# Kernel tuning notes

Hardware: AMD Instinct MI355X
Metric: run time of the kernel (lower is better)

## Reference

```python
import jax, jax.numpy as jnp
import numpy as np

N = 50000      # num nodes
E = 800000     # num edges (avg degree 16)
D = 128        # feature dim
HOP = 2        # number of propagation hops
FILL = 0.5     # self-loop fill value (A_hat = A + fill*I)


def setup_inputs() -> dict:
    key = jax.random.key(0)
    k1, k2, k3, k4, k5 = jax.random.split(key, 5)
    x_s = jax.random.normal(k1, (N, D), dtype=jnp.float32)
    x_t = jax.random.normal(k2, (N, D), dtype=jnp.float32)
    src = jax.random.randint(k3, (E,), 0, N)
    # guarantee no pre-existing self-loops so that appending all self-loops
    # exactly matches add_remaining_self_loops
    dst = (src + jax.random.randint(k4, (E,), 1, N)) % N
    edge_index = jnp.stack([src, dst]).astype(jnp.int32)
    edge_weight = jax.random.uniform(k5, (E,), dtype=jnp.float32)
    # DIMPA parameters, initialized to 1.0 per _reset_parameters
    w_s = jnp.ones((HOP + 1, 1), dtype=jnp.float32)
    w_t = jnp.ones((HOP + 1, 1), dtype=jnp.float32)
    return {"x_s": x_s, "x_t": x_t, "edge_index": edge_index,
            "edge_weight": edge_weight, "w_s": w_s, "w_t": w_t}


def _conv(x, row, col, w, n, fill):
    # Conv_Base: add self loops with weight `fill`, row-normalize by weighted
    # out-degree of `row`, scatter-add messages w_norm * x[row] onto `col`.
    loop = jnp.arange(n, dtype=row.dtype)
    row_a = jnp.concatenate([row, loop])
    col_a = jnp.concatenate([col, loop])
    w_a = jnp.concatenate([w, jnp.full((n,), fill, dtype=w.dtype)])
    deg = jax.ops.segment_sum(w_a, row_a, num_segments=n)
    deg_inv = jnp.where(deg == 0, jnp.zeros_like(deg), 1.0 / deg)  # inf -> 0
    w_norm = deg_inv[row_a] * w_a                                   # [E+n]
    return jax.ops.segment_sum(w_norm[:, None] * x[row_a], col_a, num_segments=n)


def reference(x_s, x_t, edge_index, edge_weight, w_s, w_t):
    n = x_s.shape[0]
    row, col = edge_index[0], edge_index[1]
    feat_s = w_s[0] * x_s
    feat_t = w_t[0] * x_t
    curr_s, curr_t = x_s, x_t
    for h in range(1, HOP + 1):
        curr_s = _conv(curr_s, row, col, edge_weight, n, FILL)
        # edge_index_t = edge_index[[1, 0]] -> swap row/col
        curr_t = _conv(curr_t, col, row, edge_weight, n, FILL)
        feat_s = feat_s + w_s[h] * curr_s
        feat_t = feat_t + w_t[h] * curr_t
    return jnp.concatenate([feat_s, feat_t], axis=1)  # [N, 2D]
```

## Files before the change

kernel.cpp:

```cpp
#include <hip/hip_runtime.h>

#define D 128
#define FILLV 0.5f
#define NXCD 8
#define EPT 8

#define CNT_SHIFT 22
#define DEG_MASK  0x3FFFFFu

typedef unsigned short u16;
typedef unsigned long long u64;
typedef unsigned uv4 __attribute__((ext_vector_type(4)));
typedef u64 u64v2 __attribute__((ext_vector_type(2)));
typedef u16 sv8 __attribute__((ext_vector_type(8)));

__device__ __forceinline__ u16 f2bf(float f) {
    unsigned u = __float_as_uint(f);
    u += 0x7FFF + ((u >> 16) & 1);
    return (u16)(u >> 16);
}
__device__ __forceinline__ float bf2f(u16 h) {
    return __uint_as_float(((unsigned)h) << 16);
}

__global__ void cnt_tobf_kernel(const int* __restrict__ row, const int* __restrict__ col,
                                const float* __restrict__ w,
                                unsigned* __restrict__ cnt32, unsigned* __restrict__ ranks,
                                const float* __restrict__ x_s, const float* __restrict__ x_t,
                                u16* __restrict__ xb_s, u16* __restrict__ xb_t,
                                int E, int N, int nEB, long long nd) {
    if ((int)blockIdx.x < nEB) {
        long long g  = (long long)blockIdx.x * 256 + threadIdx.x;
        long long e0 = g * EPT;
        if (e0 >= E) return;
        if (e0 + EPT <= E && (E & 3) == 0) {
            int rr[EPT]; int cc[EPT]; unsigned fx[EPT];
            #pragma unroll
            for (int h = 0; h < EPT / 4; ++h) {
                int q = (int)(e0 >> 2) + h;
                int4   r4 = *(const int4*)(row + 4 * (size_t)q);
                int4   c4 = *(const int4*)(col + 4 * (size_t)q);
                float4 w4 = *(const float4*)(w + 4 * (size_t)q);
                rr[4*h] = r4.x; rr[4*h+1] = r4.y; rr[4*h+2] = r4.z; rr[4*h+3] = r4.w;
                cc[4*h] = c4.x; cc[4*h+1] = c4.y; cc[4*h+2] = c4.z; cc[4*h+3] = c4.w;
                fx[4*h]   = (unsigned)(w4.x * 65536.0f);
                fx[4*h+1] = (unsigned)(w4.y * 65536.0f);
                fx[4*h+2] = (unsigned)(w4.z * 65536.0f);
                fx[4*h+3] = (unsigned)(w4.w * 65536.0f);
            }
            unsigned oc[EPT], orr[EPT];
            #pragma unroll
            for (int k = 0; k < EPT; ++k) {
                unsigned add = (1u << CNT_SHIFT) | fx[k];
                oc[k]  = atomicAdd(&cnt32[(size_t)cc[k]], add);
                orr[k] = atomicAdd(&cnt32[(size_t)N + rr[k]], add);
            }
            unsigned pk[EPT];
            #pragma unroll
            for (int k = 0; k < EPT; ++k)
                pk[k] = ((orr[k] >> CNT_SHIFT) << 16) | (oc[k] >> CNT_SHIFT);
            uv4 pa = {pk[0], pk[1], pk[2], pk[3]};
            uv4 pb = {pk[4], pk[5], pk[6], pk[7]};
            __builtin_nontemporal_store(pa, (uv4*)(ranks + e0));
            __builtin_nontemporal_store(pb, (uv4*)(ranks + e0 + 4));
        } else {
            for (long long e = e0; e < E && e < e0 + EPT; ++e) {
                int r = row[e], c = col[e];
                unsigned add = (1u << CNT_SHIFT) | (unsigned)(w[e] * 65536.0f);
                unsigned oc  = atomicAdd(&cnt32[(size_t)c], add);
                unsigned orr = atomicAdd(&cnt32[(size_t)N + r], add);
                ranks[e] = ((orr >> CNT_SHIFT) << 16) | (oc >> CNT_SHIFT);
            }
        }
    } else {
        long long t = (long long)(blockIdx.x - nEB) * 256 + threadIdx.x;
        long long q = nd / 4;
        const float* x; u16* xb; long long i;
        if (t < q) { x = x_s; xb = xb_s; i = t * 4; }
        else if (t < 2 * q) { x = x_t; xb = xb_t; i = (t - q) * 4; }
        else return;
        float4 v = *(const float4*)(x + i);
        ushort4 o;
        o.x = f2bf(v.x); o.y = f2bf(v.y); o.z = f2bf(v.z); o.w = f2bf(v.w);
        *(ushort4*)(xb + i) = o;
    }
}

__global__ void scanAI_kernel(unsigned* __restrict__ cnt32, float* __restrict__ dinv,
                              int* __restrict__ tsum, int total) {
    __shared__ int sh[256];
    int gid = blockIdx.x * 256 + threadIdx.x;
    int cnt = 0;
    if (gid < total) {
        unsigned v = cnt32[gid];
        float deg = (float)(v & DEG_MASK) * (1.0f / 65536.0f);
        dinv[gid] = 1.0f / (deg + FILLV);
        cnt = (int)(v >> CNT_SHIFT);
        cnt32[gid] = (unsigned)cnt;
    }
    sh[threadIdx.x] = cnt;
    __syncthreads();
    for (int off = 128; off > 0; off >>= 1) {
        if (threadIdx.x < off) sh[threadIdx.x] += sh[threadIdx.x + off];
        __syncthreads();
    }
    if (threadIdx.x == 0) tsum[blockIdx.x] = sh[0];
}

__global__ void scanC_kernel(const unsigned* __restrict__ cnt32, const int* __restrict__ tsum,
                             int* __restrict__ start, int total, int grand_total) {
    __shared__ int sh[256];
    int acc = 0;
    for (int j = threadIdx.x; j < (int)blockIdx.x; j += 256) acc += tsum[j];
    sh[threadIdx.x] = acc;
    __syncthreads();
    for (int off = 128; off > 0; off >>= 1) {
        if (threadIdx.x < off) sh[threadIdx.x] += sh[threadIdx.x + off];
        __syncthreads();
    }
    int bpref = sh[0];
    __syncthreads();
    int gid = blockIdx.x * 256 + threadIdx.x;
    int v = (gid < total) ? (int)cnt32[gid] : 0;
    sh[threadIdx.x] = v;
    __syncthreads();
    for (int off = 1; off < 256; off <<= 1) {
        int u = 0;
        if (threadIdx.x >= off) u = sh[threadIdx.x - off];
        __syncthreads();
        sh[threadIdx.x] += u;
        __syncthreads();
    }
    int run = bpref + sh[threadIdx.x] - v;
    if (gid < total) start[gid] = run;
    if (gid == 0) start[total] = grand_total;
}

__global__ void slot_kernel(const int* __restrict__ start,
                            const int* __restrict__ row, const int* __restrict__ col,
                            const float* __restrict__ w, const unsigned* __restrict__ ranks,
                            const float* __restrict__ dinv,
                            u64* __restrict__ ssst, u64* __restrict__ es, u64* __restrict__ et,
                            int E, int N) {
    long long g  = (long long)blockIdx.x * blockDim.x + threadIdx.x;
    long long e0 = g * 4;
    if (e0 >= E) return;
    if (e0 + 4 <= E && (E & 3) == 0) {
        int q = (int)(e0 >> 2);
        int4   r4 = *(const int4*)(row + 4 * (size_t)q);
        int4   c4 = *(const int4*)(col + 4 * (size_t)q);
        float4 w4 = *(const float4*)(w + 4 * (size_t)q);
        uv4    p4 = __builtin_nontemporal_load((const uv4*)(ranks + e0));
        int rr[4] = {r4.x, r4.y, r4.z, r4.w};
        int cc[4] = {c4.x, c4.y, c4.z, c4.w};
        float ww[4] = {w4.x, w4.y, w4.z, w4.w};
        unsigned pk[4] = {p4.x, p4.y, p4.z, p4.w};
        #pragma unroll
        for (int k = 0; k < 4; ++k) {
            int ss = start[cc[k]] + (int)(pk[k] & 0xffffu);
            int st = start[N + rr[k]] + (int)(pk[k] >> 16);
            float wns = ww[k] * dinv[N + rr[k]];
            float wnt = ww[k] * dinv[cc[k]];
            u64 sv = ((u64)(unsigned)st << 32) | (unsigned)ss;
            u64 ev = ((u64)__float_as_uint(wns) << 32) | (unsigned)rr[k];
            u64 tv = ((u64)__float_as_uint(wnt) << 32) | (unsigned)cc[k];
            __builtin_nontemporal_store(sv, ssst + e0 + k);
            __builtin_nontemporal_store(ev, es + e0 + k);
            __builtin_nontemporal_store(tv, et + e0 + k);
        }
    } else {
        for (long long e = e0; e < E && e < e0 + 4; ++e) {
            int r = row[e], c = col[e];
            float we = w[e];
            unsigned pk = ranks[e];
            int ss = start[c] + (int)(pk & 0xffffu);
            int st = start[N + r] + (int)(pk >> 16);
            float wns = we * dinv[N + r];
            float wnt = we * dinv[c];
            __builtin_nontemporal_store(((u64)(unsigned)st << 32) | (unsigned)ss, ssst + e);
            __builtin_nontemporal_store(((u64)__float_as_uint(wns) << 32) | (unsigned)r, es + e);
            __builtin_nontemporal_store(((u64)__float_as_uint(wnt) << 32) | (unsigned)c, et + e);
        }
    }
}

__global__ void fillX_kernel(const u64* __restrict__ ssst,
                             const u64* __restrict__ es, const u64* __restrict__ et,
                             u64* __restrict__ edges, int E, int SL) {
    long long t = (long long)(blockIdx.x >> 3) * 256 + threadIdx.x;
    long long e0 = t * 2;
    int rid = blockIdx.x & 7;
    if (e0 >= E) return;
    int lo = rid * SL, hi = lo + SL;
    if (e0 + 2 <= E) {
        u64v2 sv = __builtin_nontemporal_load((const u64v2*)(ssst + e0));
        #pragma unroll
        for (int k = 0; k < 2; ++k) {
            int ss = (int)(unsigned)(sv[k] & 0xffffffffu);
            int st = (int)(unsigned)(sv[k] >> 32);
            if ((ss >= lo) & (ss < hi)) {
                u64 ev = __builtin_nontemporal_load(es + e0 + k);
                edges[ss] = ev;
            }
            if ((st >= lo) & (st < hi)) {
                u64 tv = __builtin_nontemporal_load(et + e0 + k);
                edges[st] = tv;
            }
        }
    } else {
        u64 sv = __builtin_nontemporal_load(ssst + e0);
        int ss = (int)(unsigned)(sv & 0xffffffffu);
        int st = (int)(unsigned)(sv >> 32);
        if ((ss >= lo) & (ss < hi)) edges[ss] = __builtin_nontemporal_load(es + e0);
        if ((st >= lo) & (st < hi)) edges[st] = __builtin_nontemporal_load(et + e0);
    }
}

#define PULL_ACC4() \
    a0 += w0v*bf2f(v0[0]) + w1v*bf2f(v1[0]) + w2v*bf2f(v2[0]) + w3v*bf2f(v3[0]); \
    a1 += w0v*bf2f(v0[1]) + w1v*bf2f(v1[1]) + w2v*bf2f(v2[1]) + w3v*bf2f(v3[1]); \
    a2 += w0v*bf2f(v0[2]) + w1v*bf2f(v1[2]) + w2v*bf2f(v2[2]) + w3v*bf2f(v3[2]); \
    a3 += w0v*bf2f(v0[3]) + w1v*bf2f(v1[3]) + w2v*bf2f(v2[3]) + w3v*bf2f(v3[3]); \
    a4 += w0v*bf2f(v0[4]) + w1v*bf2f(v1[4]) + w2v*bf2f(v2[4]) + w3v*bf2f(v3[4]); \
    a5 += w0v*bf2f(v0[5]) + w1v*bf2f(v1[5]) + w2v*bf2f(v2[5]) + w3v*bf2f(v3[5]); \
    a6 += w0v*bf2f(v0[6]) + w1v*bf2f(v1[6]) + w2v*bf2f(v2[6]) + w3v*bf2f(v3[6]); \
    a7 += w0v*bf2f(v0[7]) + w1v*bf2f(v1[7]) + w2v*bf2f(v2[7]) + w3v*bf2f(v3[7]);

#define PULL_ACC2() \
    a0 += w0v*bf2f(v0[0]) + w1v*bf2f(v1[0]); a1 += w0v*bf2f(v0[1]) + w1v*bf2f(v1[1]); \
    a2 += w0v*bf2f(v0[2]) + w1v*bf2f(v1[2]); a3 += w0v*bf2f(v0[3]) + w1v*bf2f(v1[3]); \
    a4 += w0v*bf2f(v0[4]) + w1v*bf2f(v1[4]); a5 += w0v*bf2f(v0[5]) + w1v*bf2f(v1[5]); \
    a6 += w0v*bf2f(v0[6]) + w1v*bf2f(v1[6]); a7 += w0v*bf2f(v0[7]) + w1v*bf2f(v1[7]);

#define PULL_ACC1() \
    a0 += w0v*bf2f(v0[0]); a1 += w0v*bf2f(v0[1]); a2 += w0v*bf2f(v0[2]); \
    a3 += w0v*bf2f(v0[3]); a4 += w0v*bf2f(v0[4]); a5 += w0v*bf2f(v0[5]); \
    a6 += w0v*bf2f(v0[6]); a7 += w0v*bf2f(v0[7]);

#define PULL_BODY(SRC) \
    int s0 = start[wid], s1 = start[wid + 1]; \
    float a0=0.f,a1=0.f,a2=0.f,a3=0.f,a4=0.f,a5=0.f,a6=0.f,a7=0.f; \
    int k = s0; \
    for (; k + 16 <= s1; k += 16) { \
        int b = k + 4 * q; \
        int2 p0 = edges[b], p1 = edges[b+1], p2 = edges[b+2], p3 = edges[b+3]; \
        sv8 v0 = *(const sv8*)(SRC + (size_t)p0.x * D + ql * 8); \
        sv8 v1 = *(const sv8*)(SRC + (size_t)p1.x * D + ql * 8); \
        sv8 v2 = *(const sv8*)(SRC + (size_t)p2.x * D + ql * 8); \
        sv8 v3 = *(const sv8*)(SRC + (size_t)p3.x * D + ql * 8); \
        float w0v = __int_as_float(p0.y), w1v = __int_as_float(p1.y); \
        float w2v = __int_as_float(p2.y), w3v = __int_as_float(p3.y); \
        PULL_ACC4() \
    } \
    if (k + 8 <= s1) { \
        int b = k + 2 * q; \
        int2 p0 = edges[b], p1 = edges[b+1]; \
        sv8 v0 = *(const sv8*)(SRC + (size_t)p0.x * D + ql * 8); \
        sv8 v1 = *(const sv8*)(SRC + (size_t)p1.x * D + ql * 8); \
        float w0v = __int_as_float(p0.y), w1v = __int_as_float(p1.y); \
        PULL_ACC2() \
        k += 8; \
    } \
    if (k + 4 <= s1) { \
        int b = k + q; \
        int2 p0 = edges[b]; \
        sv8 v0 = *(const sv8*)(SRC + (size_t)p0.x * D + ql * 8); \
        float w0v = __int_as_float(p0.y); \
        PULL_ACC1() \
        k += 4; \
    } \
    for (; k < s1; ++k) { \
        if (q == 0) { \
            int2 p0 = edges[k]; \
            sv8 v0 = *(const sv8*)(SRC + (size_t)p0.x * D + ql * 8); \
            float w0v = __int_as_float(p0.y); \
            PULL_ACC1() \
        } \
    } \
    a0 += __shfl_xor(a0,16); a0 += __shfl_xor(a0,32); \
    a1 += __shfl_xor(a1,16); a1 += __shfl_xor(a1,32); \
    a2 += __shfl_xor(a2,16); a2 += __shfl_xor(a2,32); \
    a3 += __shfl_xor(a3,16); a3 += __shfl_xor(a3,32); \
    a4 += __shfl_xor(a4,16); a4 += __shfl_xor(a4,32); \
    a5 += __shfl_xor(a5,16); a5 += __shfl_xor(a5,32); \
    a6 += __shfl_xor(a6,16); a6 += __shfl_xor(a6,32); \
    a7 += __shfl_xor(a7,16); a7 += __shfl_xor(a7,32);

__global__ void pull1_kernel(const int* __restrict__ start, const int2* __restrict__ edges,
                             const float* __restrict__ dinv,
                             const u16* __restrict__ xb_s, const u16* __restrict__ xb_t,
                             const float* __restrict__ x_s, const float* __restrict__ x_t,
                             u16* __restrict__ ab_s, u16* __restrict__ ab_t, int N) {
    int wid0 = (int)(((long long)blockIdx.x * blockDim.x + threadIdx.x) >> 6);
    int wid = __builtin_amdgcn_readfirstlane(wid0);
    int lane = threadIdx.x & 63;
    int q = lane >> 4, ql = lane & 15;
    if (wid >= 2 * N) return;
    const u16* xb; const float* x; u16* ab; int i, o;
    if (wid < N) { i = wid;     o = N; xb = xb_s; x = x_s; ab = ab_s; }
    else         { i = wid - N; o = 0; xb = xb_t; x = x_t; ab = ab_t; }
    PULL_BODY(xb)
    if (q == 0) {
        float sw = FILLV * dinv[o + i];
        const float* xr = x + (size_t)i * D + ql * 8;
        float4 xv0 = *(const float4*)xr;
        float4 xv1 = *(const float4*)(xr + 4);
        a0 += sw * xv0.x; a1 += sw * xv0.y; a2 += sw * xv0.z; a3 += sw * xv0.w;
        a4 += sw * xv1.x; a5 += sw * xv1.y; a6 += sw * xv1.z; a7 += sw * xv1.w;
        sv8 ov;
        ov[0]=f2bf(a0); ov[1]=f2bf(a1); ov[2]=f2bf(a2); ov[3]=f2bf(a3);
        ov[4]=f2bf(a4); ov[5]=f2bf(a5); ov[6]=f2bf(a6); ov[7]=f2bf(a7);
        *(sv8*)(ab + (size_t)i * D + ql * 8) = ov;
    }
}

__global__ void pull2_kernel(const int* __restrict__ start, const int2* __restrict__ edges,
                             const float* __restrict__ dinv,
                             const u16* __restrict__ ab_s, const u16* __restrict__ ab_t,
                             const float* __restrict__ x_s, const float* __restrict__ x_t,
                             float* __restrict__ out,
                             const float* __restrict__ w_s, const float* __restrict__ w_t, int N) {
    int wid0 = (int)(((long long)blockIdx.x * blockDim.x + threadIdx.x) >> 6);
    int wid = __builtin_amdgcn_readfirstlane(wid0);
    int lane = threadIdx.x & 63;
    int q = lane >> 4, ql = lane & 15;
    if (wid >= 2 * N) return;
    const u16* ab; const float* x; const float* wv3; int i, o, hoff;
    if (wid < N) { i = wid;     o = N; ab = ab_s; x = x_s; wv3 = w_s; hoff = 0; }
    else         { i = wid - N; o = 0; ab = ab_t; x = x_t; wv3 = w_t; hoff = D; }
    PULL_BODY(ab)
    if (q == 0) {
        float sw = FILLV * dinv[o + i];
        sv8 av = *(const sv8*)(ab + (size_t)i * D + ql * 8);
        float b0=bf2f(av[0]), b1=bf2f(av[1]), b2=bf2f(av[2]), b3=bf2f(av[3]);
        float b4=bf2f(av[4]), b5=bf2f(av[5]), b6=bf2f(av[6]), b7=bf2f(av[7]);
        a0 += sw*b0; a1 += sw*b1; a2 += sw*b2; a3 += sw*b3;
        a4 += sw*b4; a5 += sw*b5; a6 += sw*b6; a7 += sw*b7;
        float w0 = wv3[0], w1 = wv3[1], w2 = wv3[2];
        const float* xr = x + (size_t)i * D + ql * 8;
        float4 xv0 = *(const float4*)xr;
        float4 xv1 = *(const float4*)(xr + 4);
        float4 o0, o1;
        o0.x = w0*xv0.x + w1*b0 + w2*a0;
        o0.y = w0*xv0.y + w1*b1 + w2*a1;
        o0.z = w0*xv0.z + w1*b2 + w2*a2;
        o0.w = w0*xv0.w + w1*b3 + w2*a3;
        o1.x = w0*xv1.x + w1*b4 + w2*a4;
        o1.y = w0*xv1.y + w1*b5 + w2*a5;
        o1.z = w0*xv1.z + w1*b6 + w2*a6;
        o1.w = w0*xv1.w + w1*b7 + w2*a7;
        float* orp = out + (size_t)i * 2 * D + hoff + ql * 8;
        *(float4*)orp = o0;
        *(float4*)(orp + 4) = o1;
    }
}

extern "C" void kernel_launch(void* const* d_in, const int* in_sizes, int n_in,
                              void* d_out, int out_size, void* d_ws, size_t ws_size,
                              hipStream_t stream) {
    const float* x_s = (const float*)d_in[0];
    const float* x_t = (const float*)d_in[1];
    const int*   ei  = (const int*)d_in[2];
    const float* ew  = (const float*)d_in[3];
    const float* w_s = (const float*)d_in[4];
    const float* w_t = (const float*)d_in[5];
    const int N = in_sizes[0] / D;
    const int E = in_sizes[3];
    const int* row = ei;
    const int* col = ei + E;

    const int total = 2 * N;
    const int nTiles = (total + 255) / 256;

    float* f      = (float*)d_ws;
    float* dinv   = f;
    int*   start  = (int*)(f + (size_t)total);
    int*   tsum   = start + (total + 2);
    char*  pc     = (char*)(tsum + 512);
    pc = (char*)(((size_t)pc + 255) & ~(size_t)255);
    u64*   edges  = (u64*)pc;
    u16*   xb_s   = (u16*)(edges + 2 * (size_t)E);
    u16*   xb_t   = xb_s + (size_t)N * D;
    u16*   ab_s   = xb_t + (size_t)N * D;
    u16*   ab_t   = ab_s + (size_t)N * D;
    unsigned* cnt32 = (unsigned*)ab_s;

    unsigned* ranks = (unsigned*)d_out;
    char* po = (char*)d_out + (((size_t)E * 4 + 15) & ~(size_t)15);
    u64* ssst = (u64*)po;
    u64* es   = ssst + (size_t)E;
    u64* et   = es + (size_t)E;
    float* out = (float*)d_out;

    hipMemsetAsync(cnt32, 0, (size_t)total * sizeof(unsigned), stream);

    long long nd = (long long)N * D;
    int blkC = (int)((nd / 2 + 255) / 256);
    int nEB  = (E + EPT * 256 - 1) / (EPT * 256);
    cnt_tobf_kernel<<<nEB + blkC, 256, 0, stream>>>(row, col, ew, cnt32, ranks,
                                                    x_s, x_t, xb_s, xb_t,
                                                    E, N, nEB, nd);
    scanAI_kernel<<<nTiles, 256, 0, stream>>>(cnt32, dinv, tsum, total);
    scanC_kernel<<<nTiles, 256, 0, stream>>>(cnt32, tsum, start, total, 2 * E);

    int blkS = (E / 4 + 256) / 256 + 1;
    slot_kernel<<<blkS, 256, 0, stream>>>(start, row, col, ew, ranks, dinv,
                                          ssst, es, et, E, N);

    int SL = ((2 * E + NXCD - 1) / NXCD + 7) & ~7;
    int blkF = (E + 511) / 512;
    fillX_kernel<<<NXCD * blkF, 256, 0, stream>>>(ssst, es, et, edges, E, SL);

    long long pull_threads = (long long)total * 64;
    int blkP = (int)((pull_threads + 255) / 256);
    pull1_kernel<<<blkP, 256, 0, stream>>>(start, (const int2*)edges, dinv, xb_s, xb_t,
                                           x_s, x_t, ab_s, ab_t, N);
    pull2_kernel<<<blkP, 256, 0, stream>>>(start, (const int2*)edges, dinv, ab_s, ab_t,
                                           x_s, x_t, out, w_s, w_t, N);
}
```

Before: 355.2 us.

## Privatize degree/count atomics per XCD and merge replicas before scan

The counting pass now picks one of eight replicated counter arrays by the hardware XCC id and uses workgroup-scope relaxed atomics. This avoids device-scope atomics contending across chiplets. A merge kernel then sums the replicas into degree and count totals and turns each replica into a per-XCD base offset. The scan adds the global start to every replica, and the slot kernel decodes an XCD tag packed into the rank bits. This adds an 8x larger memset, extra merge traffic and a 10-bit rank limit per XCD. It also relies on workgroup-scope atomics staying coherent within an XCD's L2.

```diff
diff --git a/kernel.cpp b/kernel.cpp
--- a/kernel.cpp
+++ b/kernel.cpp
@@ -22,10 +22,15 @@
 __device__ __forceinline__ float bf2f(u16 h) {
     return __uint_as_float(((unsigned)h) << 16);
 }
+__device__ __forceinline__ unsigned xcc_id() {
+    unsigned x;
+    asm volatile("s_getreg_b32 %0, hwreg(HW_REG_XCC_ID)" : "=s"(x));
+    return x & 7;
+}
 
 __global__ void cnt_tobf_kernel(const int* __restrict__ row, const int* __restrict__ col,
                                 const float* __restrict__ w,
-                                unsigned* __restrict__ cnt32, unsigned* __restrict__ ranks,
+                                unsigned* __restrict__ rep, unsigned* __restrict__ ranks,
                                 const float* __restrict__ x_s, const float* __restrict__ x_t,
                                 u16* __restrict__ xb_s, u16* __restrict__ xb_t,
                                 int E, int N, int nEB, long long nd) {
@@ -33,6 +38,9 @@
         long long g  = (long long)blockIdx.x * 256 + threadIdx.x;
         long long e0 = g * EPT;
         if (e0 >= E) return;
+        unsigned x = xcc_id();
+        size_t base = (size_t)x * (2u * (unsigned)N);
+        unsigned xtag = x << 10;
         if (e0 + EPT <= E && (E & 3) == 0) {
             int rr[EPT]; int cc[EPT]; unsigned fx[EPT];
             #pragma unroll
@@ -52,13 +60,15 @@
             #pragma unroll
             for (int k = 0; k < EPT; ++k) {
                 unsigned add = (1u << CNT_SHIFT) | fx[k];
-                oc[k]  = atomicAdd(&cnt32[(size_t)cc[k]], add);
-                orr[k] = atomicAdd(&cnt32[(size_t)N + rr[k]], add);
+                oc[k]  = __hip_atomic_fetch_add(&rep[base + (unsigned)cc[k]], add,
+                                                __ATOMIC_RELAXED, __HIP_MEMORY_SCOPE_WORKGROUP);
+                orr[k] = __hip_atomic_fetch_add(&rep[base + (unsigned)N + (unsigned)rr[k]], add,
+                                                __ATOMIC_RELAXED, __HIP_MEMORY_SCOPE_WORKGROUP);
             }
             unsigned pk[EPT];
             #pragma unroll
             for (int k = 0; k < EPT; ++k)
-                pk[k] = ((orr[k] >> CNT_SHIFT) << 16) | (oc[k] >> CNT_SHIFT);
+                pk[k] = ((xtag | (orr[k] >> CNT_SHIFT)) << 16) | (xtag | (oc[k] >> CNT_SHIFT));
             uv4 pa = {pk[0], pk[1], pk[2], pk[3]};
             uv4 pb = {pk[4], pk[5], pk[6], pk[7]};
             __builtin_nontemporal_store(pa, (uv4*)(ranks + e0));
@@ -67,9 +77,11 @@
             for (long long e = e0; e < E && e < e0 + EPT; ++e) {
                 int r = row[e], c = col[e];
                 unsigned add = (1u << CNT_SHIFT) | (unsigned)(w[e] * 65536.0f);
-                unsigned oc  = atomicAdd(&cnt32[(size_t)c], add);
-                unsigned orr = atomicAdd(&cnt32[(size_t)N + r], add);
-                ranks[e] = ((orr >> CNT_SHIFT) << 16) | (oc >> CNT_SHIFT);
+                unsigned oc  = __hip_atomic_fetch_add(&rep[base + (unsigned)c], add,
+                                                      __ATOMIC_RELAXED, __HIP_MEMORY_SCOPE_WORKGROUP);
+                unsigned orr = __hip_atomic_fetch_add(&rep[base + (unsigned)N + (unsigned)r], add,
+                                                      __ATOMIC_RELAXED, __HIP_MEMORY_SCOPE_WORKGROUP);
+                ranks[e] = ((xtag | (orr >> CNT_SHIFT)) << 16) | (xtag | (oc >> CNT_SHIFT));
             }
         }
     } else {
@@ -86,19 +98,29 @@
     }
 }
 
-__global__ void scanAI_kernel(unsigned* __restrict__ cnt32, float* __restrict__ dinv,
-                              int* __restrict__ tsum, int total) {
+__global__ void mergeAI_kernel(unsigned* __restrict__ rep, float* __restrict__ dinv,
+                               unsigned* __restrict__ cnttot, int* __restrict__ tsum,
+                               int total) {
     __shared__ int sh[256];
     int gid = blockIdx.x * 256 + threadIdx.x;
-    int cnt = 0;
+    int tot = 0;
     if (gid < total) {
-        unsigned v = cnt32[gid];
-        float deg = (float)(v & DEG_MASK) * (1.0f / 65536.0f);
+        unsigned v[NXCD];
+        #pragma unroll
+        for (int x = 0; x < NXCD; ++x) v[x] = rep[(size_t)x * total + gid];
+        unsigned run = 0, degsum = 0;
+        #pragma unroll
+        for (int x = 0; x < NXCD; ++x) {
+            degsum += v[x] & DEG_MASK;
+            rep[(size_t)x * total + gid] = run;
+            run += v[x] >> CNT_SHIFT;
+        }
+        tot = (int)run;
+        float deg = (float)degsum * (1.0f / 65536.0f);
         dinv[gid] = 1.0f / (deg + FILLV);
-        cnt = (int)(v >> CNT_SHIFT);
-        cnt32[gid] = (unsigned)cnt;
-    }
-    sh[threadIdx.x] = cnt;
+        cnttot[gid] = run;
+    }
+    sh[threadIdx.x] = tot;
     __syncthreads();
     for (int off = 128; off > 0; off >>= 1) {
         if (threadIdx.x < off) sh[threadIdx.x] += sh[threadIdx.x + off];
@@ -107,7 +129,8 @@
     if (threadIdx.x == 0) tsum[blockIdx.x] = sh[0];
 }
 
-__global__ void scanC_kernel(const unsigned* __restrict__ cnt32, const int* __restrict__ tsum,
+__global__ void scanC_kernel(const unsigned* __restrict__ cnttot, const int* __restrict__ tsum,
+                             unsigned* __restrict__ rep,
                              int* __restrict__ start, int total, int grand_total) {
     __shared__ int sh[256];
     int acc = 0;
@@ -121,7 +144,7 @@
     int bpref = sh[0];
     __syncthreads();
     int gid = blockIdx.x * 256 + threadIdx.x;
-    int v = (gid < total) ? (int)cnt32[gid] : 0;
+    int v = (gid < total) ? (int)cnttot[gid] : 0;
     sh[threadIdx.x] = v;
     __syncthreads();
     for (int off = 1; off < 256; off <<= 1) {
@@ -132,16 +155,21 @@
         __syncthreads();
     }
     int run = bpref + sh[threadIdx.x] - v;
-    if (gid < total) start[gid] = run;
+    if (gid < total) {
+        start[gid] = run;
+        #pragma unroll
+        for (int x = 0; x < NXCD; ++x) rep[(size_t)x * total + gid] += (unsigned)run;
+    }
     if (gid == 0) start[total] = grand_total;
 }
 
-__global__ void slot_kernel(const int* __restrict__ start,
+__global__ void slot_kernel(const unsigned* __restrict__ rep,
                             const int* __restrict__ row, const int* __restrict__ col,
                             const float* __restrict__ w, const unsigned* __restrict__ ranks,
                             const float* __restrict__ dinv,
                             u64* __restrict__ ssst, u64* __restrict__ es, u64* __restrict__ et,
                             int E, int N) {
+    const int total = 2 * N;
     long long g  = (long long)blockIdx.x * blockDim.x + threadIdx.x;
     long long e0 = g * 4;
     if (e0 >= E) return;
@@ -157,8 +185,9 @@
         unsigned pk[4] = {p4.x, p4.y, p4.z, p4.w};
         #pragma unroll
         for (int k = 0; k < 4; ++k) {
-            int ss = start[cc[k]] + (int)(pk[k] & 0xffffu);
-            int st = start[N + rr[k]] + (int)(pk[k] >> 16);
+            unsigned pks = pk[k] & 0xffffu, pkt = pk[k] >> 16;
+            int ss = (int)(rep[(size_t)(pks >> 10) * total + cc[k]] + (pks & 0x3ffu));
+            int st = (int)(rep[(size_t)(pkt >> 10) * total + (size_t)N + rr[k]] + (pkt & 0x3ffu));
             float wns = ww[k] * dinv[N + rr[k]];
             float wnt = ww[k] * dinv[cc[k]];
             u64 sv = ((u64)(unsigned)st << 32) | (unsigned)ss;
@@ -173,8 +202,9 @@
             int r = row[e], c = col[e];
             float we = w[e];
             unsigned pk = ranks[e];
-            int ss = start[c] + (int)(pk & 0xffffu);
-            int st = start[N + r] + (int)(pk >> 16);
+            unsigned pks = pk & 0xffffu, pkt = pk >> 16;
+            int ss = (int)(rep[(size_t)(pks >> 10) * total + c] + (pks & 0x3ffu));
+            int st = (int)(rep[(size_t)(pkt >> 10) * total + (size_t)N + r] + (pkt & 0x3ffu));
             float wns = we * dinv[N + r];
             float wnt = we * dinv[c];
             __builtin_nontemporal_store(((u64)(unsigned)st << 32) | (unsigned)ss, ssst + e);
@@ -383,7 +413,8 @@
     u16*   xb_t   = xb_s + (size_t)N * D;
     u16*   ab_s   = xb_t + (size_t)N * D;
     u16*   ab_t   = ab_s + (size_t)N * D;
-    unsigned* cnt32 = (unsigned*)ab_s;
+    unsigned* rep    = (unsigned*)ab_s;
+    unsigned* cnttot = rep + (size_t)NXCD * total;
 
     unsigned* ranks = (unsigned*)d_out;
     char* po = (char*)d_out + (((size_t)E * 4 + 15) & ~(size_t)15);
@@ -392,19 +423,19 @@
     u64* et   = es + (size_t)E;
     float* out = (float*)d_out;
 
-    hipMemsetAsync(cnt32, 0, (size_t)total * sizeof(unsigned), stream);
+    hipMemsetAsync(rep, 0, (size_t)NXCD * total * sizeof(unsigned), stream);
 
     long long nd = (long long)N * D;
     int blkC = (int)((nd / 2 + 255) / 256);
     int nEB  = (E + EPT * 256 - 1) / (EPT * 256);
-    cnt_tobf_kernel<<<nEB + blkC, 256, 0, stream>>>(row, col, ew, cnt32, ranks,
+    cnt_tobf_kernel<<<nEB + blkC, 256, 0, stream>>>(row, col, ew, rep, ranks,
                                                     x_s, x_t, xb_s, xb_t,
                                                     E, N, nEB, nd);
-    scanAI_kernel<<<nTiles, 256, 0, stream>>>(cnt32, dinv, tsum, total);
-    scanC_kernel<<<nTiles, 256, 0, stream>>>(cnt32, tsum, start, total, 2 * E);
+    mergeAI_kernel<<<nTiles, 256, 0, stream>>>(rep, dinv, cnttot, tsum, total);
+    scanC_kernel<<<nTiles, 256, 0, stream>>>(cnttot, tsum, rep, start, total, 2 * E);
 
     int blkS = (E / 4 + 256) / 256 + 1;
-    slot_kernel<<<blkS, 256, 0, stream>>>(start, row, col, ew, ranks, dinv,
+    slot_kernel<<<blkS, 256, 0, stream>>>(rep, row, col, ew, ranks, dinv,
                                           ssst, es, et, E, N);
 
     int SL = ((2 * E + NXCD - 1) / NXCD + 7) & ~7;
```

After: 358.5 us. No clear change (+0.9%).
